# Performance work log

Hardware: AMD Instinct MI355X
Metric: run time of the kernel (lower is better)

Reference implementation:

```python
import jax, jax.numpy as jnp
import numpy as np

B, T, C, D = 4, 4096, 1024, 64

def setup_inputs() -> dict:
    key = jax.random.key(0)
    k1, k2, k3, k4 = jax.random.split(key, 4)
    return {
        "x": jax.random.normal(k1, (B, T, C), dtype=jnp.float32),
        "Wq": jax.random.normal(k2, (C, D), dtype=jnp.float32) * (C ** -0.5),
        "Wk": jax.random.normal(k3, (C, D), dtype=jnp.float32) * (C ** -0.5),
        "Wv": jax.random.normal(k4, (C, D), dtype=jnp.float32) * (C ** -0.5),
    }

def reference(x, Wq, Wk, Wv):
    # Single-head causal self-attention (context defaults to x; dropout p=0 -> identity)
    T_ = x.shape[1]
    Q = jnp.einsum('btc,cd->btd', x, Wq)
    K = jnp.einsum('btc,cd->btd', x, Wk)
    V = jnp.einsum('btc,cd->btd', x, Wv)
    scores = jnp.einsum('btd,bsd->bts', Q, K) / jnp.sqrt(jnp.float32(K.shape[-1]))
    causal = jnp.tril(jnp.ones((T_, T_), dtype=bool))  # [T, T]
    scores = jnp.where(causal, scores, -jnp.inf)
    attn = jax.nn.softmax(scores, axis=-1)
    out = jnp.einsum('bts,bsd->btd', attn, V)
    return out
```

## Files before the change

### kernel.cpp

```cpp
#include <hip/hip_runtime.h>

typedef short bf16x8 __attribute__((ext_vector_type(8)));
typedef float f32x4 __attribute__((ext_vector_type(4)));
typedef float f32x16 __attribute__((ext_vector_type(16)));
typedef unsigned short u16;
typedef unsigned int u32;

#define MFMA_BF16 __builtin_amdgcn_mfma_f32_16x16x32_bf16
#define MFMA32 __builtin_amdgcn_mfma_f32_32x32x16_bf16

static __device__ __forceinline__ u16 f2bf(float f) {
  union { float f; unsigned u; } v; v.f = f;
  return (u16)((v.u + 0x7FFFu + ((v.u >> 16) & 1u)) >> 16);
}
static __device__ __forceinline__ u32 cvtpk(float lo, float hi) {
  u32 r;
  asm("v_cvt_pk_bf16_f32 %0, %1, %2" : "=v"(r) : "v"(lo), "v"(hi));
  return r;
}
static __device__ __forceinline__ bf16x8 cvt8(uint4 p, uint4 q) {
  union { u32 w[4]; bf16x8 b; } r;
  r.w[0] = cvtpk(__uint_as_float(p.x), __uint_as_float(p.y));
  r.w[1] = cvtpk(__uint_as_float(p.z), __uint_as_float(p.w));
  r.w[2] = cvtpk(__uint_as_float(q.x), __uint_as_float(q.y));
  r.w[3] = cvtpk(__uint_as_float(q.z), __uint_as_float(q.w));
  return r.b;
}
static __device__ __forceinline__ float xhalf(float x) { return __shfl_xor(x, 32); }
static __device__ __forceinline__ u32 xhalfu(u32 x) { return (u32)__shfl_xor((int)x, 32); }

static __device__ __forceinline__ void gload16(const void* g, void* l) {
  __builtin_amdgcn_global_load_lds(
      (const __attribute__((address_space(1))) u32*)g,
      (__attribute__((address_space(3))) u32*)l, 16, 0, 0);
}

__global__ __launch_bounds__(256) void wt_kernel(const float* __restrict__ Wq,
                                                 const float* __restrict__ Wk,
                                                 const float* __restrict__ Wv,
                                                 u16* __restrict__ Wt) {
  const int nrow = blockIdx.x;
  const int m = nrow >> 6, n = nrow & 63;
  const float* W = (m == 0) ? Wq : ((m == 1) ? Wk : Wv);
  const float s = (m == 0) ? 0.125f * 1.44269504f : 1.0f;
  for (int k = threadIdx.x; k < 1024; k += 256)
    Wt[(size_t)nrow * 1024 + k] = f2bf(W[(size_t)k * 64 + n] * s);
}

__global__ __launch_bounds__(256) void qkv6(const float* __restrict__ x,
                                            const u16* __restrict__ Wt,
                                            u16* __restrict__ Qb,
                                            u16* __restrict__ Kb,
                                            u16* __restrict__ Vt) {
  __shared__ __align__(16) char sh[2][32 * 1024];
  const int w = threadIdx.x >> 6, l = threadIdx.x & 63;
  const int lane16 = l & 15, laneHi = l >> 4;
  const int r0 = blockIdx.x * 32;
  const int nt0 = w * 3;

  const f32x4 fzero = {0.f, 0.f, 0.f, 0.f};
  f32x4 acc0 = fzero, acc1 = fzero, acc2 = fzero;
  f32x4 acc3 = fzero, acc4 = fzero, acc5 = fzero;

  auto stage = [&](int buf, int s) {
    char* base = &sh[buf][0];
    const int k0 = s * 64;
    if (w < 3) {
#pragma unroll
      for (int ii = 0; ii < 8; ++ii) {
        const int nt = w * 4 + (ii >> 1), kh = ii & 1;
        const u16* g = Wt + (size_t)(nt * 16 + lane16) * 1024 + k0 + kh * 32 + laneHi * 8;
        gload16(g, base + (nt * 2 + kh) * 1024);
      }
    } else {
#pragma unroll
      for (int ii = 0; ii < 8; ++ii) {
        const int m = ii >> 2, kh = (ii >> 1) & 1, p = ii & 1;
        const float* g = x + (size_t)(r0 + m * 16 + lane16) * 1024 + k0 + kh * 32 + laneHi * 8 + p * 4;
        gload16(g, base + (24 + ii) * 1024);
      }
    }
  };

  auto comp = [&](int buf) {
    const char* base = &sh[buf][0] + (size_t)l * 16;
    bf16x8 b00 = *(const bf16x8*)(base + ((nt0 + 0) * 2 + 0) * 1024);
    bf16x8 b01 = *(const bf16x8*)(base + ((nt0 + 0) * 2 + 1) * 1024);
    bf16x8 b10 = *(const bf16x8*)(base + ((nt0 + 1) * 2 + 0) * 1024);
    bf16x8 b11 = *(const bf16x8*)(base + ((nt0 + 1) * 2 + 1) * 1024);
    bf16x8 b20 = *(const bf16x8*)(base + ((nt0 + 2) * 2 + 0) * 1024);
    bf16x8 b21 = *(const bf16x8*)(base + ((nt0 + 2) * 2 + 1) * 1024);
    uint4 x00a = *(const uint4*)(base + 24 * 1024);
    uint4 x00b = *(const uint4*)(base + 25 * 1024);
    uint4 x01a = *(const uint4*)(base + 26 * 1024);
    uint4 x01b = *(const uint4*)(base + 27 * 1024);
    uint4 x10a = *(const uint4*)(base + 28 * 1024);
    uint4 x10b = *(const uint4*)(base + 29 * 1024);
    uint4 x11a = *(const uint4*)(base + 30 * 1024);
    uint4 x11b = *(const uint4*)(base + 31 * 1024);
    bf16x8 a00 = cvt8(x00a, x00b);
    bf16x8 a01 = cvt8(x01a, x01b);
    bf16x8 a10 = cvt8(x10a, x10b);
    bf16x8 a11 = cvt8(x11a, x11b);
    acc0 = MFMA_BF16(a00, b00, acc0, 0, 0, 0);
    acc0 = MFMA_BF16(a01, b01, acc0, 0, 0, 0);
    acc1 = MFMA_BF16(a00, b10, acc1, 0, 0, 0);
    acc1 = MFMA_BF16(a01, b11, acc1, 0, 0, 0);
    acc2 = MFMA_BF16(a00, b20, acc2, 0, 0, 0);
    acc2 = MFMA_BF16(a01, b21, acc2, 0, 0, 0);
    acc3 = MFMA_BF16(a10, b00, acc3, 0, 0, 0);
    acc3 = MFMA_BF16(a11, b01, acc3, 0, 0, 0);
    acc4 = MFMA_BF16(a10, b10, acc4, 0, 0, 0);
    acc4 = MFMA_BF16(a11, b11, acc4, 0, 0, 0);
    acc5 = MFMA_BF16(a10, b20, acc5, 0, 0, 0);
    acc5 = MFMA_BF16(a11, b21, acc5, 0, 0, 0);
  };

  stage(0, 0);
  __syncthreads();
#pragma unroll 1
  for (int s = 0; s < 16; ++s) {
    if (s + 1 < 16) stage((s + 1) & 1, s + 1);
    comp(s & 1);
    __syncthreads();
  }

#define ST(AC, m, i)                                                        \
  {                                                                         \
    const int nt = nt0 + (i);                                               \
    if (nt < 4) {                                                           \
      _Pragma("unroll")                                                     \
      for (int r = 0; r < 4; ++r)                                           \
        Qb[(size_t)(r0 + (m) * 16 + laneHi * 4 + r) * 64 + nt * 16 + lane16] = f2bf(AC[r]); \
    } else if (nt < 8) {                                                    \
      _Pragma("unroll")                                                     \
      for (int r = 0; r < 4; ++r)                                           \
        Kb[(size_t)(r0 + (m) * 16 + laneHi * 4 + r) * 64 + (nt - 4) * 16 + lane16] = f2bf(AC[r]); \
    } else {                                                                \
      const int d = (nt - 8) * 16 + lane16;                                 \
      uint2 v;                                                              \
      v.x = cvtpk(AC[0], AC[1]);                                            \
      v.y = cvtpk(AC[2], AC[3]);                                            \
      *(uint2*)(Vt + ((size_t)(r0 >> 5) * 64 + d) * 32 + (m) * 16 + laneHi * 4) = v; \
    }                                                                       \
  }

  ST(acc0, 0, 0) ST(acc1, 0, 1) ST(acc2, 0, 2)
  ST(acc3, 1, 0) ST(acc4, 1, 1) ST(acc5, 1, 2)
}

__global__ __launch_bounds__(256) void attn7(const u16* __restrict__ Qb,
                                             const u16* __restrict__ Kb,
                                             const u16* __restrict__ Vt,
                                             float* __restrict__ out) {
  __shared__ float shC[3][64][37];
  __shared__ __align__(16) float shT[32][68];

  const int tid = threadIdx.x, w = tid >> 6, l = tid & 63;
  const int q = l & 31, hi = l >> 5;
  const bool isHi = hi != 0;
  const int b = blockIdx.x & 3;
  const int j = blockIdx.x >> 2;
  const int t = (j >> 6) ? (j & 63) : (127 - (j & 63));
  const int q0 = t * 32, bT = b * 4096;

  const u16* qp = Qb + (size_t)(bT + q0 + q) * 64 + 8 * hi;
  const bf16x8 qf0 = *(const bf16x8*)(qp);
  const bf16x8 qf1 = *(const bf16x8*)(qp + 16);
  const bf16x8 qf2 = *(const bf16x8*)(qp + 32);
  const bf16x8 qf3 = *(const bf16x8*)(qp + 48);

  const int nu = t + 1;
  const int s = (nu * w) >> 2, e = (nu * (w + 1)) >> 2;

  f32x16 o0 = {}, o1 = {};
  float m = -INFINITY, lsum = 0.f;

  bf16x8 kA[4], vA[4], kB[4], vB[4];

  auto loadKV = [&](bf16x8 (&kf)[4], bf16x8 (&vf)[4], int u) {
    const int k0 = bT + u * 32;
    const u16* kp = Kb + (size_t)(k0 + q) * 64 + 8 * hi;
#pragma unroll
    for (int kc = 0; kc < 4; ++kc) kf[kc] = *(const bf16x8*)(kp + kc * 16);
    const u16* vbase = Vt + (size_t)(b * 128 + u) * 2048;
#pragma unroll
    for (int dt = 0; dt < 2; ++dt)
#pragma unroll
      for (int c = 0; c < 2; ++c)
        vf[dt * 2 + c] = *(const bf16x8*)(vbase + (dt * 32 + q) * 32 + c * 16 + 8 * hi);
  };

  auto compute = [&](bf16x8 (&kf)[4], bf16x8 (&vf)[4], int u) {
    f32x16 sc = {};
    __builtin_amdgcn_s_setprio(1);
    sc = MFMA32(kf[0], qf0, sc, 0, 0, 0);
    sc = MFMA32(kf[1], qf1, sc, 0, 0, 0);
    sc = MFMA32(kf[2], qf2, sc, 0, 0, 0);
    sc = MFMA32(kf[3], qf3, sc, 0, 0, 0);
    __builtin_amdgcn_s_setprio(0);

    if (u == t) {
#pragma unroll
      for (int r = 0; r < 16; ++r) {
        const int key = (r & 3) + 8 * (r >> 2) + 4 * hi;
        if (key > q) sc[r] = -INFINITY;
      }
    }

    float pm = sc[0];
#pragma unroll
    for (int r = 1; r < 16; ++r) pm = fmaxf(pm, sc[r]);
    pm = fmaxf(pm, xhalf(pm));

    if (!__all(pm <= m + 8.f)) {
      const float mn = fmaxf(m, pm);
      const float al = exp2f(fmaxf(m - mn, -80.f));
#pragma unroll
      for (int r = 0; r < 16; ++r) { o0[r] *= al; o1[r] *= al; }
      lsum *= al;
      m = mn;
    }

    float p[16];
    float rs = 0.f;
#pragma unroll
    for (int r = 0; r < 16; ++r) { p[r] = exp2f(sc[r] - m); rs += p[r]; }
    rs += xhalf(rs);
    lsum += rs;

    u32 wl0 = cvtpk(p[0], p[1]),  wl1 = cvtpk(p[2], p[3]);
    u32 wh0 = cvtpk(p[4], p[5]),  wh1 = cvtpk(p[6], p[7]);
    u32 yl0 = cvtpk(p[8], p[9]),  yl1 = cvtpk(p[10], p[11]);
    u32 yh0 = cvtpk(p[12], p[13]), yh1 = cvtpk(p[14], p[15]);
    u32 sl0 = xhalfu(wl0), sl1 = xhalfu(wl1);
    u32 sh0 = xhalfu(wh0), sh1 = xhalfu(wh1);
    u32 tl0 = xhalfu(yl0), tl1 = xhalfu(yl1);
    u32 th0 = xhalfu(yh0), th1 = xhalfu(yh1);
    union { u32 w4[4]; bf16x8 v; } pf0, pf1;
    pf0.w4[0] = isHi ? sh0 : wl0;
    pf0.w4[1] = isHi ? sh1 : wl1;
    pf0.w4[2] = isHi ? wh0 : sl0;
    pf0.w4[3] = isHi ? wh1 : sl1;
    pf1.w4[0] = isHi ? th0 : yl0;
    pf1.w4[1] = isHi ? th1 : yl1;
    pf1.w4[2] = isHi ? yh0 : tl0;
    pf1.w4[3] = isHi ? yh1 : tl1;

    __builtin_amdgcn_s_setprio(1);
    o0 = MFMA32(vf[0], pf0.v, o0, 0, 0, 0);
    o0 = MFMA32(vf[1], pf1.v, o0, 0, 0, 0);
    o1 = MFMA32(vf[2], pf0.v, o1, 0, 0, 0);
    o1 = MFMA32(vf[3], pf1.v, o1, 0, 0, 0);
    __builtin_amdgcn_s_setprio(0);
  };

  int u = s;
  if (u < e) loadKV(kA, vA, u);
#pragma unroll 1
  while (u < e) {
    if (u + 1 < e) loadKV(kB, vB, u + 1);
    compute(kA, vA, u);
    ++u;
    if (u >= e) break;
    if (u + 1 < e) loadKV(kA, vA, u + 1);
    compute(kB, vB, u);
    ++u;
  }

  if (w > 0) {
    float* dst = &shC[w - 1][l][0];
    dst[0] = m; dst[1] = lsum;
#pragma unroll
    for (int r = 0; r < 16; ++r) { dst[2 + r] = o0[r]; dst[18 + r] = o1[r]; }
  }
  __syncthreads();
  if (w == 0) {
#pragma unroll
    for (int peer = 0; peer < 3; ++peer) {
      const float* src = &shC[peer][l][0];
      const float pm = src[0], pl = src[1];
      const float mn = fmaxf(m, pm);
      const float aS = exp2f(fmaxf(m - mn, -80.f));
      const float aP = exp2f(fmaxf(pm - mn, -80.f));
      m = mn;
      lsum = lsum * aS + pl * aP;
#pragma unroll
      for (int r = 0; r < 16; ++r) {
        o0[r] = o0[r] * aS + src[2 + r] * aP;
        o1[r] = o1[r] * aS + src[18 + r] * aP;
      }
    }
    const float inv = 1.0f / lsum;
#pragma unroll
    for (int r = 0; r < 16; ++r) {
      const int d = (r & 3) + 8 * (r >> 2) + 4 * hi;
      shT[q][d] = o0[r] * inv;
      shT[q][32 + d] = o1[r] * inv;
    }
    __asm volatile("s_waitcnt lgkmcnt(0)" ::: "memory");
#pragma unroll
    for (int it = 0; it < 8; ++it) {
      const int row = it * 4 + (l >> 4);
      const int c4 = (l & 15) * 4;
      float4 v = *(const float4*)&shT[row][c4];
      *(float4*)(out + (size_t)(bT + q0 + row) * 64 + c4) = v;
    }
  }
}

extern "C" void kernel_launch(void* const* d_in, const int* in_sizes, int n_in,
                              void* d_out, int out_size, void* d_ws, size_t ws_size,
                              hipStream_t stream) {
  const float* x  = (const float*)d_in[0];
  const float* Wq = (const float*)d_in[1];
  const float* Wk = (const float*)d_in[2];
  const float* Wv = (const float*)d_in[3];
  float* out = (float*)d_out;

  char* ws = (char*)d_ws;
  u16* Wt = (u16*)ws;
  u16* Qb = (u16*)(ws + 393216);
  u16* Kb = (u16*)(ws + 393216 + 2097152);
  u16* Vt = (u16*)(ws + 393216 + 2 * 2097152);

  wt_kernel<<<192, 256, 0, stream>>>(Wq, Wk, Wv, Wt);
  qkv6<<<512, 256, 0, stream>>>(x, Wt, Qb, Kb, Vt);
  attn7<<<512, 256, 0, stream>>>(Qb, Kb, Vt, out);
}
```

Before: 77.11 us.

## Process 64-key blocks per attention iteration with interleaved score MFMAs

The attention loop now handles two 32-key sub-tiles per iteration (64 keys), which halves the iteration count. It also interleaves two independent MFMA accumulation chains for QK^T and for PV, and runs the softmax max and sum as tree reductions over both tiles. This is meant to cut per-iteration overhead (online-softmax rescale checks, cross-lane shuffles, loop control) and expose more instruction-level parallelism. In exchange, register pressure doubles for the K/V prefetch buffers, which risks lower occupancy or spills, and the split of work across waves becomes coarser, so load balance between waves may suffer.

New measurement: 87.50 us. 1.13x slower.

```diff
diff --git a/kernel.cpp b/kernel.cpp
--- a/kernel.cpp
+++ b/kernel.cpp
@@ -149,7 +149,7 @@
   ST(acc3, 1, 0) ST(acc4, 1, 1) ST(acc5, 1, 2)
 }
 
-__global__ __launch_bounds__(256) void attn7(const u16* __restrict__ Qb,
+__global__ __launch_bounds__(256) void attn8(const u16* __restrict__ Qb,
                                              const u16* __restrict__ Kb,
                                              const u16* __restrict__ Vt,
                                              float* __restrict__ out) {
@@ -170,47 +170,56 @@
   const bf16x8 qf2 = *(const bf16x8*)(qp + 32);
   const bf16x8 qf3 = *(const bf16x8*)(qp + 48);
 
-  const int nu = t + 1;
+  const int nu = (t + 2) >> 1;
   const int s = (nu * w) >> 2, e = (nu * (w + 1)) >> 2;
 
   f32x16 o0 = {}, o1 = {};
   float m = -INFINITY, lsum = 0.f;
 
-  bf16x8 kA[4], vA[4], kB[4], vB[4];
-
-  auto loadKV = [&](bf16x8 (&kf)[4], bf16x8 (&vf)[4], int u) {
-    const int k0 = bT + u * 32;
-    const u16* kp = Kb + (size_t)(k0 + q) * 64 + 8 * hi;
-#pragma unroll
-    for (int kc = 0; kc < 4; ++kc) kf[kc] = *(const bf16x8*)(kp + kc * 16);
-    const u16* vbase = Vt + (size_t)(b * 128 + u) * 2048;
-#pragma unroll
-    for (int dt = 0; dt < 2; ++dt)
-#pragma unroll
-      for (int c = 0; c < 2; ++c)
-        vf[dt * 2 + c] = *(const bf16x8*)(vbase + (dt * 32 + q) * 32 + c * 16 + 8 * hi);
+  bf16x8 kA[8], vA[8], kB[8], vB[8];
+
+  auto loadKV = [&](bf16x8 (&kf)[8], bf16x8 (&vf)[8], int u) {
+#pragma unroll
+    for (int s2 = 0; s2 < 2; ++s2) {
+      const int k0 = bT + u * 64 + s2 * 32;
+      const u16* kp = Kb + (size_t)(k0 + q) * 64 + 8 * hi;
+#pragma unroll
+      for (int kc = 0; kc < 4; ++kc) kf[s2 * 4 + kc] = *(const bf16x8*)(kp + kc * 16);
+      const u16* vbase = Vt + (size_t)(b * 128 + u * 2 + s2) * 2048;
+#pragma unroll
+      for (int dt = 0; dt < 2; ++dt)
+#pragma unroll
+        for (int c = 0; c < 2; ++c)
+          vf[s2 * 4 + dt * 2 + c] = *(const bf16x8*)(vbase + (dt * 32 + q) * 32 + c * 16 + 8 * hi);
+    }
   };
 
-  auto compute = [&](bf16x8 (&kf)[4], bf16x8 (&vf)[4], int u) {
-    f32x16 sc = {};
+  auto compute = [&](bf16x8 (&kf)[8], bf16x8 (&vf)[8], int u) {
+    f32x16 sc0 = {}, sc1 = {};
     __builtin_amdgcn_s_setprio(1);
-    sc = MFMA32(kf[0], qf0, sc, 0, 0, 0);
-    sc = MFMA32(kf[1], qf1, sc, 0, 0, 0);
-    sc = MFMA32(kf[2], qf2, sc, 0, 0, 0);
-    sc = MFMA32(kf[3], qf3, sc, 0, 0, 0);
+    sc0 = MFMA32(kf[0], qf0, sc0, 0, 0, 0);  sc1 = MFMA32(kf[4], qf0, sc1, 0, 0, 0);
+    sc0 = MFMA32(kf[1], qf1, sc0, 0, 0, 0);  sc1 = MFMA32(kf[5], qf1, sc1, 0, 0, 0);
+    sc0 = MFMA32(kf[2], qf2, sc0, 0, 0, 0);  sc1 = MFMA32(kf[6], qf2, sc1, 0, 0, 0);
+    sc0 = MFMA32(kf[3], qf3, sc0, 0, 0, 0);  sc1 = MFMA32(kf[7], qf3, sc1, 0, 0, 0);
     __builtin_amdgcn_s_setprio(0);
 
-    if (u == t) {
+    if (u == nu - 1) {
 #pragma unroll
       for (int r = 0; r < 16; ++r) {
         const int key = (r & 3) + 8 * (r >> 2) + 4 * hi;
-        if (key > q) sc[r] = -INFINITY;
+        if (u * 64 + key > q0 + q) sc0[r] = -INFINITY;
+        if (u * 64 + 32 + key > q0 + q) sc1[r] = -INFINITY;
       }
     }
 
-    float pm = sc[0];
-#pragma unroll
-    for (int r = 1; r < 16; ++r) pm = fmaxf(pm, sc[r]);
+    float mx[16];
+#pragma unroll
+    for (int r = 0; r < 16; ++r) mx[r] = fmaxf(sc0[r], sc1[r]);
+#pragma unroll
+    for (int r = 0; r < 8; ++r) mx[r] = fmaxf(mx[r], mx[r + 8]);
+#pragma unroll
+    for (int r = 0; r < 4; ++r) mx[r] = fmaxf(mx[r], mx[r + 4]);
+    float pm = fmaxf(fmaxf(mx[0], mx[1]), fmaxf(mx[2], mx[3]));
     pm = fmaxf(pm, xhalf(pm));
 
     if (!__all(pm <= m + 8.f)) {
@@ -222,36 +231,56 @@
       m = mn;
     }
 
-    float p[16];
-    float rs = 0.f;
-#pragma unroll
-    for (int r = 0; r < 16; ++r) { p[r] = exp2f(sc[r] - m); rs += p[r]; }
+    float p0[16], p1[16], sm[16];
+#pragma unroll
+    for (int r = 0; r < 16; ++r) {
+      p0[r] = exp2f(sc0[r] - m);
+      p1[r] = exp2f(sc1[r] - m);
+      sm[r] = p0[r] + p1[r];
+    }
+#pragma unroll
+    for (int r = 0; r < 8; ++r) sm[r] += sm[r + 8];
+#pragma unroll
+    for (int r = 0; r < 4; ++r) sm[r] += sm[r + 4];
+    float rs = (sm[0] + sm[1]) + (sm[2] + sm[3]);
     rs += xhalf(rs);
     lsum += rs;
 
-    u32 wl0 = cvtpk(p[0], p[1]),  wl1 = cvtpk(p[2], p[3]);
-    u32 wh0 = cvtpk(p[4], p[5]),  wh1 = cvtpk(p[6], p[7]);
-    u32 yl0 = cvtpk(p[8], p[9]),  yl1 = cvtpk(p[10], p[11]);
-    u32 yh0 = cvtpk(p[12], p[13]), yh1 = cvtpk(p[14], p[15]);
-    u32 sl0 = xhalfu(wl0), sl1 = xhalfu(wl1);
-    u32 sh0 = xhalfu(wh0), sh1 = xhalfu(wh1);
-    u32 tl0 = xhalfu(yl0), tl1 = xhalfu(yl1);
-    u32 th0 = xhalfu(yh0), th1 = xhalfu(yh1);
-    union { u32 w4[4]; bf16x8 v; } pf0, pf1;
-    pf0.w4[0] = isHi ? sh0 : wl0;
-    pf0.w4[1] = isHi ? sh1 : wl1;
-    pf0.w4[2] = isHi ? wh0 : sl0;
-    pf0.w4[3] = isHi ? wh1 : sl1;
-    pf1.w4[0] = isHi ? th0 : yl0;
-    pf1.w4[1] = isHi ? th1 : yl1;
-    pf1.w4[2] = isHi ? yh0 : tl0;
-    pf1.w4[3] = isHi ? yh1 : tl1;
+    union { u32 w4[4]; bf16x8 v; } pf0a, pf1a, pf0b, pf1b;
+    {
+      u32 wl0 = cvtpk(p0[0], p0[1]),  wl1 = cvtpk(p0[2], p0[3]);
+      u32 wh0 = cvtpk(p0[4], p0[5]),  wh1 = cvtpk(p0[6], p0[7]);
+      u32 yl0 = cvtpk(p0[8], p0[9]),  yl1 = cvtpk(p0[10], p0[11]);
+      u32 yh0 = cvtpk(p0[12], p0[13]), yh1 = cvtpk(p0[14], p0[15]);
+      u32 sl0 = xhalfu(wl0), sl1 = xhalfu(wl1);
+      u32 sh0 = xhalfu(wh0), sh1 = xhalfu(wh1);
+      u32 tl0 = xhalfu(yl0), tl1 = xhalfu(yl1);
+      u32 th0 = xhalfu(yh0), th1 = xhalfu(yh1);
+      pf0a.w4[0] = isHi ? sh0 : wl0;  pf0a.w4[1] = isHi ? sh1 : wl1;
+      pf0a.w4[2] = isHi ? wh0 : sl0;  pf0a.w4[3] = isHi ? wh1 : sl1;
+      pf1a.w4[0] = isHi ? th0 : yl0;  pf1a.w4[1] = isHi ? th1 : yl1;
+      pf1a.w4[2] = isHi ? yh0 : tl0;  pf1a.w4[3] = isHi ? yh1 : tl1;
+    }
+    {
+      u32 wl0 = cvtpk(p1[0], p1[1]),  wl1 = cvtpk(p1[2], p1[3]);
+      u32 wh0 = cvtpk(p1[4], p1[5]),  wh1 = cvtpk(p1[6], p1[7]);
+      u32 yl0 = cvtpk(p1[8], p1[9]),  yl1 = cvtpk(p1[10], p1[11]);
+      u32 yh0 = cvtpk(p1[12], p1[13]), yh1 = cvtpk(p1[14], p1[15]);
+      u32 sl0 = xhalfu(wl0), sl1 = xhalfu(wl1);
+      u32 sh0 = xhalfu(wh0), sh1 = xhalfu(wh1);
+      u32 tl0 = xhalfu(yl0), tl1 = xhalfu(yl1);
+      u32 th0 = xhalfu(yh0), th1 = xhalfu(yh1);
+      pf0b.w4[0] = isHi ? sh0 : wl0;  pf0b.w4[1] = isHi ? sh1 : wl1;
+      pf0b.w4[2] = isHi ? wh0 : sl0;  pf0b.w4[3] = isHi ? wh1 : sl1;
+      pf1b.w4[0] = isHi ? th0 : yl0;  pf1b.w4[1] = isHi ? th1 : yl1;
+      pf1b.w4[2] = isHi ? yh0 : tl0;  pf1b.w4[3] = isHi ? yh1 : tl1;
+    }
 
     __builtin_amdgcn_s_setprio(1);
-    o0 = MFMA32(vf[0], pf0.v, o0, 0, 0, 0);
-    o0 = MFMA32(vf[1], pf1.v, o0, 0, 0, 0);
-    o1 = MFMA32(vf[2], pf0.v, o1, 0, 0, 0);
-    o1 = MFMA32(vf[3], pf1.v, o1, 0, 0, 0);
+    o0 = MFMA32(vf[0], pf0a.v, o0, 0, 0, 0);  o1 = MFMA32(vf[2], pf0a.v, o1, 0, 0, 0);
+    o0 = MFMA32(vf[1], pf1a.v, o0, 0, 0, 0);  o1 = MFMA32(vf[3], pf1a.v, o1, 0, 0, 0);
+    o0 = MFMA32(vf[4], pf0b.v, o0, 0, 0, 0);  o1 = MFMA32(vf[6], pf0b.v, o1, 0, 0, 0);
+    o0 = MFMA32(vf[5], pf1b.v, o0, 0, 0, 0);  o1 = MFMA32(vf[7], pf1b.v, o1, 0, 0, 0);
     __builtin_amdgcn_s_setprio(0);
   };
 
@@ -326,5 +355,5 @@
 
   wt_kernel<<<192, 256, 0, stream>>>(Wq, Wk, Wv, Wt);
   qkv6<<<512, 256, 0, stream>>>(x, Wt, Qb, Kb, Vt);
-  attn7<<<512, 256, 0, stream>>>(Qb, Kb, Vt, out);
-}
+  attn8<<<512, 256, 0, stream>>>(Qb, Kb, Vt, out);
+}
```
